# Kernel optimization log

Measured on AMD Instinct MI355X. Metric: run time of the kernel, lower is better.

Reference implementation:

```python
import jax, jax.numpy as jnp
import numpy as np

S_SRC, S_TGT, B = 64, 48, 2048
SRC, TGT, E, H = 256, 256, 512, 1024
NEG = -1e30  # stands in for -inf mask on pad/start classes (identical softmax in fp32)


def setup_inputs() -> dict:
    key = jax.random.key(0)
    ks = jax.random.split(key, 16)
    def p(k, shape):
        return jax.random.normal(k, shape, jnp.float32) * 0.02
    # padding_idx=0 -> embedding row 0 is zeros
    enc_emb = p(ks[0], (SRC, E)).at[0].set(0.0)
    dec_emb = p(ks[1], (TGT, E)).at[0].set(0.0)
    return {
        "src_seq": jax.random.randint(ks[2], (S_SRC, B), 1, SRC),
        "tgt_seq": jax.random.randint(ks[3], (S_TGT, B), 2, TGT),
        "enc_emb": enc_emb,
        "enc_Wih": p(ks[4], (3 * H, E)),
        "enc_Whh": p(ks[5], (3 * H, H)),
        "enc_bih": p(ks[6], (3 * H,)),
        "enc_bhh": p(ks[7], (3 * H,)),
        "dec_emb": dec_emb,
        "dec_Wih": p(ks[8], (3 * H, E)),
        "dec_Whh": p(ks[9], (3 * H, H)),
        "dec_bih": p(ks[10], (3 * H,)),
        "dec_bhh": p(ks[11], (3 * H,)),
        "unemb_W": p(ks[12], (TGT - 2, H)),
        "unemb_b": p(ks[13], (TGT - 2,)),
    }


def gru(x, h0, Wih, Whh, bih, bhh):
    """PyTorch-convention GRU. x: [S,B,E], h0: [B,H]. Gate order r,z,n."""
    xp = jnp.einsum('sbe,ge->sbg', x, Wih) + bih  # input projections for all steps
    def step(h, xt):
        gh = h @ Whh.T + bhh
        xr, xz, xn = jnp.split(xt, 3, axis=-1)
        hr, hz, hn = jnp.split(gh, 3, axis=-1)
        r = jax.nn.sigmoid(xr + hr)
        z = jax.nn.sigmoid(xz + hz)
        n = jnp.tanh(xn + r * hn)
        h = (1 - z) * n + z * h
        return h, h
    hT, hs = jax.lax.scan(step, h0, xp)
    return hs, hT  # [S,B,H], [B,H]


def reference(src_seq, tgt_seq, enc_emb, enc_Wih, enc_Whh, enc_bih, enc_bhh,
              dec_emb, dec_Wih, dec_Whh, dec_bih, dec_bhh, unemb_W, unemb_b):
    # ---- Encoder ----
    x0 = enc_emb[src_seq]                                   # [S_src, B, E]
    h0 = jnp.zeros((src_seq.shape[1], H), x0.dtype)
    _, h = gru(x0, h0, enc_Wih, enc_Whh, enc_bih, enc_bhh)  # [B, H]
    # ---- Decoder (training / teacher-forced path) ----
    xd = dec_emb[tgt_seq]                                   # [S_tgt, B, E]
    xs, _ = gru(xd, h, dec_Wih, dec_Whh, dec_bih, dec_bhh)  # [S_tgt, B, H]
    seq_out = jnp.einsum('sbh,vh->sbv', xs, unemb_W) + unemb_b  # [S_tgt, B, TGT-2]
    mask_cols = jnp.full(seq_out.shape[:-1] + (2,), NEG, seq_out.dtype)
    logits = jnp.concatenate([mask_cols, seq_out], axis=-1)     # [S_tgt, B, TGT]
    # labels shifted left by one; last position = 0 (ignore_index)
    labels = jnp.concatenate([tgt_seq[1:], jnp.zeros_like(tgt_seq[:1])], axis=0)
    logp = jax.nn.log_softmax(logits, axis=-1)
    nll = -jnp.take_along_axis(logp, labels[..., None], axis=-1)[..., 0]
    valid = (labels != 0).astype(nll.dtype)
    return jnp.sum(nll * valid) / jnp.sum(valid)
```

## Files before the change

### kernel.cpp

```cpp
#include <hip/hip_runtime.h>
#include <math.h>

typedef unsigned short ushort_t;
typedef __attribute__((ext_vector_type(8))) short short8;
typedef __attribute__((ext_vector_type(4))) float f32x4;

#define Bn 2048
#define Hn 1024
#define En 512
#define NSLOT 9

__device__ __forceinline__ float sigmoidf_(float x) { return 1.f / (1.f + expf(-x)); }

__device__ __forceinline__ ushort_t bf16rn(float f) {
  unsigned u = __float_as_uint(f);
  return (ushort_t)((u + 0x7FFFu + ((u >> 16) & 1u)) >> 16);
}

__device__ __forceinline__ float bf2f(ushort_t u) {
  return __uint_as_float(((unsigned)u) << 16);
}

__global__ __launch_bounds__(256) void cvt_bf16_kernel(const float* __restrict__ in,
                                                       ushort_t* __restrict__ out, int n4) {
  int i = blockIdx.x * 256 + threadIdx.x;
  if (i < n4) {
    float4 v = ((const float4*)in)[i];
    ushort4 o;
    o.x = bf16rn(v.x); o.y = bf16rn(v.y); o.z = bf16rn(v.z); o.w = bf16rn(v.w);
    ((ushort4*)out)[i] = o;
  }
}

__global__ __launch_bounds__(256) void cvt_pad_wu_kernel(const float* __restrict__ src,
                                                         ushort_t* __restrict__ dst) {
  int i = blockIdx.x * 256 + threadIdx.x;
  if (i < 256 * Hn / 4) {
    float4 v = make_float4(0.f, 0.f, 0.f, 0.f);
    if (i * 4 < 254 * Hn) v = ((const float4*)src)[i];
    ushort4 o;
    o.x = bf16rn(v.x); o.y = bf16rn(v.y); o.z = bf16rn(v.z); o.w = bf16rn(v.w);
    ((ushort4*)dst)[i] = o;
  }
}

#define GLOAD(gsrc, ldst)                                                      \
  __builtin_amdgcn_global_load_lds(                                            \
      (const __attribute__((address_space(1))) unsigned int*)(gsrc),           \
      (__attribute__((address_space(3))) unsigned int*)(ldst), 16, 0, 0)

#define PIPE_BAR(N)                                                            \
  asm volatile("s_waitcnt vmcnt(" #N ")" ::: "memory");                        \
  __builtin_amdgcn_s_barrier();                                                \
  __builtin_amdgcn_sched_barrier(0);

#define SWZ(ROW, C) ((C) ^ (((ROW) >> 1) & 3))
#define SWZ64(ROW, C) ((C) ^ ((ROW) & 7))

__global__ __launch_bounds__(256) void pgemm_kernel(
    const ushort_t* __restrict__ A,
    const ushort_t* __restrict__ Bw,
    const float* __restrict__ bias,
    float* __restrict__ P)
{
  __shared__ __align__(16) ushort_t As[64 * 32];
  __shared__ __align__(16) ushort_t Bs[64 * 32];

  const int tid = threadIdx.x;
  const int lane = tid & 63;
  const int wid = tid >> 6;
  const int wr = wid >> 1, wc = wid & 1;
  const int m0 = blockIdx.x * 64;
  const int n0 = blockIdx.y * 64;

  const int srow = tid >> 2;
  const int sseg = SWZ(srow, tid & 3) * 8;
  const ushort_t* aP = A + (size_t)(m0 + srow) * En + sseg;
  const ushort_t* bP = Bw + (size_t)(n0 + srow) * En + sseg;

  const int kc = lane >> 4;
  const int ra0 = wr * 32 + (lane & 15), ra1 = ra0 + 16;
  const int rb0 = wc * 32 + (lane & 15), rb1 = rb0 + 16;
  const int aoff0 = ra0 * 32 + SWZ(ra0, kc) * 8;
  const int aoff1 = ra1 * 32 + SWZ(ra1, kc) * 8;
  const int boff0 = rb0 * 32 + SWZ(rb0, kc) * 8;
  const int boff1 = rb1 * 32 + SWZ(rb1, kc) * 8;

  const f32x4 zero = {0.f, 0.f, 0.f, 0.f};
  f32x4 acc[2][2] = {{zero, zero}, {zero, zero}};

  for (int k0 = 0; k0 < En; k0 += 32) {
    GLOAD(aP + k0, &As[wid * 512]);
    GLOAD(bP + k0, &Bs[wid * 512]);
    asm volatile("s_waitcnt vmcnt(0)" ::: "memory");
    __syncthreads();
    short8 a0 = *(const short8*)&As[aoff0];
    short8 a1 = *(const short8*)&As[aoff1];
    short8 b0 = *(const short8*)&Bs[boff0];
    short8 b1 = *(const short8*)&Bs[boff1];
    acc[0][0] = __builtin_amdgcn_mfma_f32_16x16x32_bf16(a0, b0, acc[0][0], 0, 0, 0);
    acc[0][1] = __builtin_amdgcn_mfma_f32_16x16x32_bf16(a0, b1, acc[0][1], 0, 0, 0);
    acc[1][0] = __builtin_amdgcn_mfma_f32_16x16x32_bf16(a1, b0, acc[1][0], 0, 0, 0);
    acc[1][1] = __builtin_amdgcn_mfma_f32_16x16x32_bf16(a1, b1, acc[1][1], 0, 0, 0);
    __syncthreads();
  }

  const int colb = n0 + wc * 32 + (lane & 15);
  const int rowb = m0 + wr * 32 + ((lane >> 4) << 2);
#pragma unroll
  for (int j = 0; j < 2; ++j) {
    const int g = colb + j * 16;
    const float bv = bias[g];
#pragma unroll
    for (int i = 0; i < 2; ++i)
#pragma unroll
      for (int reg = 0; reg < 4; ++reg)
        P[(size_t)(rowb + i * 16 + reg) * 3072 + g] = acc[i][j][reg] + bv;
  }
}

#define KSTEP(BUF)                                                             \
  {                                                                            \
    short8 aF[2][2], bF[3][2];                                                 \
    _Pragma("unroll") for (int fi = 0; fi < 2; ++fi)                           \
        _Pragma("unroll") for (int h = 0; h < 2; ++h)                          \
            aF[fi][h] = *(const short8*)&As[BUF][aoff[fi][h]];                 \
    _Pragma("unroll") for (int g = 0; g < 3; ++g)                              \
        _Pragma("unroll") for (int h = 0; h < 2; ++h)                          \
            bF[g][h] = *(const short8*)&Bs[BUF][g][boff[h]];                   \
    __builtin_amdgcn_s_setprio(1);                                             \
    _Pragma("unroll") for (int h = 0; h < 2; ++h)                              \
        _Pragma("unroll") for (int g = 0; g < 3; ++g)                          \
            _Pragma("unroll") for (int fi = 0; fi < 2; ++fi)                   \
                acc[g][fi] = __builtin_amdgcn_mfma_f32_16x16x32_bf16(          \
                    aF[fi][h], bF[g][h], acc[g][fi], 0, 0, 0);                 \
    __builtin_amdgcn_s_setprio(0);                                             \
  }

#define GSTAGE(BUF, T)                                                         \
  {                                                                            \
    const int k0_ = (T) * 64;                                                  \
    GLOAD(aSrc + k0_, &As[BUF][wid * 512]);                                    \
    GLOAD(bSrc0 + k0_, &Bs[BUF][0][wid * 512]);                                \
    GLOAD(bSrc1 + k0_, &Bs[BUF][1][wid * 512]);                                \
    GLOAD(bSrc2 + k0_, &Bs[BUF][2][wid * 512]);                                \
  }

__global__ __launch_bounds__(512, 4) void gru_step_mfma(
    const int* __restrict__ seq_row,
    const float* __restrict__ P,
    const ushort_t* __restrict__ Whh,
    const float* __restrict__ bhh,
    const ushort_t* __restrict__ h_in_b,
    ushort_t* __restrict__ h_out_b)
{
  __shared__ __align__(16) ushort_t As[2][64 * 64];
  __shared__ __align__(16) ushort_t Bs[2][3][64 * 64];
  __shared__ int toks[64];

  const int tid = threadIdx.x;
  const int lane = tid & 63;
  const int wid = tid >> 6;
  const int wr = wid & 1;
  const int wc = wid >> 1;

  const int bid = blockIdx.x;
  const int q = bid & 7, t_ = bid >> 3;
  const int n0 = ((q << 1) | (t_ & 1)) * 64;
  const int m0 = (t_ >> 1) * 64;

  if (tid < 64) toks[tid] = seq_row[m0 + tid];
  __syncthreads();

  const int srow = tid >> 3;
  const int sseg = SWZ64(srow, tid & 7) * 8;

  const ushort_t* aSrc  = h_in_b + (size_t)(m0 + srow) * Hn + sseg;
  const ushort_t* bSrc0 = Whh + (size_t)(0 * Hn + n0 + srow) * Hn + sseg;
  const ushort_t* bSrc1 = Whh + (size_t)(1 * Hn + n0 + srow) * Hn + sseg;
  const ushort_t* bSrc2 = Whh + (size_t)(2 * Hn + n0 + srow) * Hn + sseg;

  const int kc = lane >> 4;
  int aoff[2][2], boff[2];
#pragma unroll
  for (int fi = 0; fi < 2; ++fi) {
    const int ra = wr * 32 + fi * 16 + (lane & 15);
#pragma unroll
    for (int h = 0; h < 2; ++h) aoff[fi][h] = ra * 64 + SWZ64(ra, h * 4 + kc) * 8;
  }
  {
    const int rb = wc * 16 + (lane & 15);
#pragma unroll
    for (int h = 0; h < 2; ++h) boff[h] = rb * 64 + SWZ64(rb, h * 4 + kc) * 8;
  }

  const f32x4 zero = {0.f, 0.f, 0.f, 0.f};
  f32x4 acc[3][2];
#pragma unroll
  for (int g = 0; g < 3; ++g)
#pragma unroll
    for (int fi = 0; fi < 2; ++fi) acc[g][fi] = zero;

  GSTAGE(0, 0);
  int buf = 0;
  for (int t = 0; t < 15; ++t) {
    GSTAGE(buf ^ 1, t + 1);
    PIPE_BAR(4)
    KSTEP(buf)
    buf ^= 1;
  }
  PIPE_BAR(0)
  KSTEP(buf)

  const int n = n0 + wc * 16 + (lane & 15);
  const int rowl = wr * 32 + ((lane >> 4) << 2);
  const float bhr = bhh[n];
  const float bhz = bhh[Hn + n];
  const float bhn = bhh[2 * Hn + n];
#pragma unroll
  for (int fi = 0; fi < 2; ++fi) {
#pragma unroll
    for (int reg = 0; reg < 4; ++reg) {
      const int lr = rowl + fi * 16 + reg;
      const int m = m0 + lr;
      const float* prow = P + (size_t)toks[lr] * 3072;
      const float xr = prow[n];
      const float xz = prow[Hn + n];
      const float xn = prow[2 * Hn + n];
      const float r = sigmoidf_(xr + acc[0][fi][reg] + bhr);
      const float z = sigmoidf_(xz + acc[1][fi][reg] + bhz);
      const float nn = tanhf(xn + r * (acc[2][fi][reg] + bhn));
      const float hv = bf2f(h_in_b[(size_t)m * Hn + n]);
      const float o = (1.f - z) * nn + z * hv;
      h_out_b[(size_t)m * Hn + n] = bf16rn(o);
    }
  }
}

#define USTAGE(BUF, T)                                                         \
  {                                                                            \
    const int k0_ = (T) * 32;                                                  \
    if (uwid < 2) GLOAD(ha + k0_, AsU(BUF) + (tid >> 2) * 32);                 \
    GLOAD(w0 + k0_, BsU(BUF) + 0 * 2048 + uwid * 512);                         \
    GLOAD(w1 + k0_, BsU(BUF) + 1 * 2048 + uwid * 512);                         \
    GLOAD(w2 + k0_, BsU(BUF) + 2 * 2048 + uwid * 512);                         \
    GLOAD(w3 + k0_, BsU(BUF) + 3 * 2048 + uwid * 512);                         \
  }

#define UPIPE_BAR(N01, N23)                                                    \
  {                                                                            \
    if (uwid < 2) { asm volatile("s_waitcnt vmcnt(" #N01 ")" ::: "memory"); }  \
    else          { asm volatile("s_waitcnt vmcnt(" #N23 ")" ::: "memory"); }  \
    __builtin_amdgcn_s_barrier();                                              \
    __builtin_amdgcn_sched_barrier(0);                                         \
  }

#define UKSTEP(BUF)                                                            \
  {                                                                            \
    short8 a_[2], b_[4];                                                       \
    _Pragma("unroll") for (int fi = 0; fi < 2; ++fi)                           \
        a_[fi] = *(const short8*)(AsU(BUF) + uaoff[fi]);                       \
    _Pragma("unroll") for (int fj = 0; fj < 4; ++fj)                           \
        b_[fj] = *(const short8*)(BsU(BUF) + uboff[fj]);                       \
    _Pragma("unroll") for (int fi = 0; fi < 2; ++fi)                           \
        _Pragma("unroll") for (int fj = 0; fj < 4; ++fj)                       \
            acc[fi][fj] = __builtin_amdgcn_mfma_f32_16x16x32_bf16(             \
                a_[fi], b_[fj], acc[fi][fj], 0, 0, 0);                         \
  }

__global__ __launch_bounds__(256) void unembed_batched(
    const ushort_t* __restrict__ hseq,
    int s0,
    const ushort_t* __restrict__ Wp,
    const float* __restrict__ bu,
    const int* __restrict__ tgt_seq,
    double* __restrict__ loss_acc,
    unsigned long long* __restrict__ cnt_acc)
{
  __shared__ __align__(16) char usmem[36 * 1024];
#define AsU(BUF) ((ushort_t*)usmem + (BUF) * 1024)
#define BsU(BUF) ((ushort_t*)(usmem + 4 * 1024) + (BUF) * 8192)
  float* lg = (float*)usmem;

  const int tid = threadIdx.x;
  const int lane = tid & 63;
  const int uwid = tid >> 6;

  const int step = blockIdx.x >> 6;
  const int slot = (s0 + step) % NSLOT;
  const int m0 = (blockIdx.x & 63) * 32;
  const ushort_t* h_b = hseq + (size_t)slot * Bn * Hn;
  const int* labels = tgt_seq + (size_t)(s0 + step + 1) * Bn;

  const int srow = tid >> 2;
  const int sseg = SWZ(srow, tid & 3) * 8;

  const ushort_t* ha = h_b + (size_t)(m0 + srow) * Hn + sseg;
  const ushort_t* w0 = Wp + (size_t)(0 * 64 + srow) * Hn + sseg;
  const ushort_t* w1 = Wp + (size_t)(1 * 64 + srow) * Hn + sseg;
  const ushort_t* w2 = Wp + (size_t)(2 * 64 + srow) * Hn + sseg;
  const ushort_t* w3 = Wp + (size_t)(3 * 64 + srow) * Hn + sseg;

  const int kc = lane >> 4;
  int uaoff[2], uboff[4];
#pragma unroll
  for (int fi = 0; fi < 2; ++fi) {
    const int ra = fi * 16 + (lane & 15);
    uaoff[fi] = ra * 32 + SWZ(ra, kc) * 8;
  }
#pragma unroll
  for (int fj = 0; fj < 4; ++fj) {
    const int rb = uwid * 64 + fj * 16 + (lane & 15);
    uboff[fj] = rb * 32 + SWZ(rb, kc) * 8;
  }

  const f32x4 zero = {0.f, 0.f, 0.f, 0.f};
  f32x4 acc[2][4];
#pragma unroll
  for (int fi = 0; fi < 2; ++fi)
#pragma unroll
    for (int fj = 0; fj < 4; ++fj) acc[fi][fj] = zero;

  USTAGE(0, 0);
  int buf = 0;
  for (int t = 0; t < 31; ++t) {
    USTAGE(buf ^ 1, t + 1);
    UPIPE_BAR(5, 4)
    UKSTEP(buf)
    buf ^= 1;
  }
  UPIPE_BAR(0, 0)
  UKSTEP(buf)

  __syncthreads();
#pragma unroll
  for (int fj = 0; fj < 4; ++fj) {
    const int col = uwid * 64 + fj * 16 + (lane & 15);
    const float bv = (col < 254) ? bu[col] : 0.f;
#pragma unroll
    for (int fi = 0; fi < 2; ++fi) {
#pragma unroll
      for (int reg = 0; reg < 4; ++reg) {
        const int row = fi * 16 + (lane >> 4) * 4 + reg;
        lg[row * 256 + col] = (col < 254) ? (acc[fi][fj][reg] + bv) : -1e30f;
      }
    }
  }
  __syncthreads();

  float wsum = 0.f;
  int wcnt = 0;
#pragma unroll
  for (int rr = 0; rr < 8; ++rr) {
    const int r = uwid * 8 + rr;
    const float4 v4 = *(const float4*)&lg[r * 256 + lane * 4];
    float mx = fmaxf(fmaxf(v4.x, v4.y), fmaxf(v4.z, v4.w));
    for (int o = 32; o > 0; o >>= 1) mx = fmaxf(mx, __shfl_xor(mx, o));
    float s = expf(v4.x - mx) + expf(v4.y - mx) + expf(v4.z - mx) + expf(v4.w - mx);
    for (int o = 32; o > 0; o >>= 1) s += __shfl_xor(s, o);
    if (lane == 0) {
      const int lab = labels[m0 + r];
      if (lab != 0) {
        wsum += (logf(s) + mx) - lg[r * 256 + lab - 2];
        wcnt += 1;
      }
    }
  }
  if (lane == 0) {
    atomicAdd(loss_acc, (double)wsum);
    atomicAdd(cnt_acc, (unsigned long long)wcnt);
  }
}

__global__ void finalize_kernel(const double* __restrict__ loss_acc,
                                const unsigned long long* __restrict__ cnt_acc,
                                unsigned* __restrict__ out)
{
  unsigned long long cnt = cnt_acc[0];
  if (cnt == 0ull) cnt = 1ull;
  const float f = (float)(loss_acc[0] / (double)cnt);
  const unsigned u = __float_as_uint(f);
  const unsigned bf = (u + 0x7FFFu + ((u >> 16) & 1u)) >> 16;
  out[0] = (u & 0xFFFF0000u) | (bf & 0xFFFFu);
}

extern "C" void kernel_launch(void* const* d_in, const int* in_sizes, int n_in,
                              void* d_out, int out_size, void* d_ws, size_t ws_size,
                              hipStream_t stream)
{
  const int* src_seq = (const int*)d_in[0];
  const int* tgt_seq = (const int*)d_in[1];
  const float* enc_emb = (const float*)d_in[2];
  const float* enc_Wih = (const float*)d_in[3];
  const float* enc_Whh = (const float*)d_in[4];
  const float* enc_bih = (const float*)d_in[5];
  const float* enc_bhh = (const float*)d_in[6];
  const float* dec_emb = (const float*)d_in[7];
  const float* dec_Wih = (const float*)d_in[8];
  const float* dec_Whh = (const float*)d_in[9];
  const float* dec_bih = (const float*)d_in[10];
  const float* dec_bhh = (const float*)d_in[11];
  const float* unemb_W = (const float*)d_in[12];
  const float* unemb_b = (const float*)d_in[13];

  char* p = (char*)d_ws;
  ushort_t* hseq = (ushort_t*)p; p += (size_t)NSLOT * Bn * Hn * 2;
  ushort_t* eWih = (ushort_t*)p; p += (size_t)3 * Hn * En * 2;
  ushort_t* eWhh = (ushort_t*)p; p += (size_t)3 * Hn * Hn * 2;
  ushort_t* dWih = (ushort_t*)p; p += (size_t)3 * Hn * En * 2;
  ushort_t* dWhh = (ushort_t*)p; p += (size_t)3 * Hn * Hn * 2;
  ushort_t* eEmb = (ushort_t*)p; p += (size_t)256 * En * 2;
  ushort_t* dEmb = (ushort_t*)p; p += (size_t)256 * En * 2;
  ushort_t* Wp   = (ushort_t*)p; p += (size_t)256 * Hn * 2;
  float* Pe = (float*)p; p += (size_t)256 * 3072 * 4;
  float* Pd = (float*)p; p += (size_t)256 * 3072 * 4;
  double* loss_acc = (double*)p;
  unsigned long long* cnt_acc = (unsigned long long*)(p + 8);

  ushort_t* slot7 = hseq + (size_t)7 * Bn * Hn;
  ushort_t* slot8 = hseq + (size_t)8 * Bn * Hn;

  hipMemsetAsync(slot7, 0, (size_t)Bn * Hn * 2, stream);
  hipMemsetAsync(loss_acc, 0, 16, stream);

  struct { const float* src; ushort_t* dst; int n; } cv[6] = {
      {enc_Wih, eWih, 3 * Hn * En}, {enc_Whh, eWhh, 3 * Hn * Hn},
      {dec_Wih, dWih, 3 * Hn * En}, {dec_Whh, dWhh, 3 * Hn * Hn},
      {enc_emb, eEmb, 256 * En},    {dec_emb, dEmb, 256 * En}};
  for (int i = 0; i < 6; ++i) {
    int n4 = cv[i].n / 4;
    cvt_bf16_kernel<<<(n4 + 255) / 256, 256, 0, stream>>>(cv[i].src, cv[i].dst, n4);
  }
  cvt_pad_wu_kernel<<<(256 * Hn / 4 + 255) / 256, 256, 0, stream>>>(unemb_W, Wp);

  {
    const dim3 pg(4, 48);
    pgemm_kernel<<<pg, 256, 0, stream>>>(eEmb, eWih, enc_bih, Pe);
    pgemm_kernel<<<pg, 256, 0, stream>>>(dEmb, dWih, dec_bih, Pd);
  }

  const ushort_t* in_b = slot7;
  for (int s = 0; s < 64; ++s) {
    ushort_t* out_b = (s & 1) ? slot7 : slot8;
    gru_step_mfma<<<512, 512, 0, stream>>>(src_seq + (size_t)s * Bn, Pe, eWhh, enc_bhh,
                                           in_b, out_b);
    in_b = out_b;
  }

  int done = 0;
  for (int s = 0; s < 47; ++s) {
    const ushort_t* din_b = (s == 0) ? slot7 : hseq + (size_t)((s - 1) % NSLOT) * Bn * Hn;
    ushort_t* dout_b = hseq + (size_t)(s % NSLOT) * Bn * Hn;
    gru_step_mfma<<<512, 512, 0, stream>>>(tgt_seq + (size_t)s * Bn, Pd, dWhh, dec_bhh,
                                           din_b, dout_b);
    if (s == 7 || s == 15 || s == 23 || s == 31 || s == 39 || s == 46) {
      const int cnt = s + 1 - done;
      unembed_batched<<<cnt * 64, 256, 0, stream>>>(hseq, done, Wp, unemb_b, tgt_seq,
                                                    loss_acc, cnt_acc);
      done = s + 1;
    }
  }

  finalize_kernel<<<1, 1, 0, stream>>>(loss_acc, cnt_acc, (unsigned*)d_out);
}
```

Baseline: 2.593 ms.

## Process two timesteps per unembed block with 64-wide K tiles and 8 waves

The unembedding kernel now handles a pair of decoder timesteps per block (64 rows of h), using 512 threads arranged as 2x4 waves and a K-tile of 64 instead of 32. Each staged slice of the weight matrix is therefore reused across twice as many rows, and there are half as many pipeline iterations and barriers. It also raises MFMA priority with s_setprio and skips atomics from waves with no contributions. The cost is higher LDS use (80KB) per block, fewer blocks in flight, and an odd-count tail where half the block does redundant work.

```diff
diff --git a/kernel.cpp b/kernel.cpp
--- a/kernel.cpp
+++ b/kernel.cpp
@@ -239,79 +239,83 @@
 
 #define USTAGE(BUF, T)                                                         \
   {                                                                            \
-    const int k0_ = (T) * 32;                                                  \
-    if (uwid < 2) GLOAD(ha + k0_, AsU(BUF) + (tid >> 2) * 32);                 \
-    GLOAD(w0 + k0_, BsU(BUF) + 0 * 2048 + uwid * 512);                         \
-    GLOAD(w1 + k0_, BsU(BUF) + 1 * 2048 + uwid * 512);                         \
-    GLOAD(w2 + k0_, BsU(BUF) + 2 * 2048 + uwid * 512);                         \
-    GLOAD(w3 + k0_, BsU(BUF) + 3 * 2048 + uwid * 512);                         \
-  }
-
-#define UPIPE_BAR(N01, N23)                                                    \
-  {                                                                            \
-    if (uwid < 2) { asm volatile("s_waitcnt vmcnt(" #N01 ")" ::: "memory"); }  \
-    else          { asm volatile("s_waitcnt vmcnt(" #N23 ")" ::: "memory"); }  \
-    __builtin_amdgcn_s_barrier();                                              \
-    __builtin_amdgcn_sched_barrier(0);                                         \
+    const int k0_ = (T) * 64;                                                  \
+    GLOAD(ha + k0_, AsU(BUF) + wid * 512);                                     \
+    GLOAD(w0 + k0_, BsU(BUF) + 0 * 4096 + wid * 512);                          \
+    GLOAD(w1 + k0_, BsU(BUF) + 1 * 4096 + wid * 512);                          \
+    GLOAD(w2 + k0_, BsU(BUF) + 2 * 4096 + wid * 512);                          \
+    GLOAD(w3 + k0_, BsU(BUF) + 3 * 4096 + wid * 512);                          \
   }
 
 #define UKSTEP(BUF)                                                            \
   {                                                                            \
-    short8 a_[2], b_[4];                                                       \
+    short8 a_[2][2], b_[4][2];                                                 \
     _Pragma("unroll") for (int fi = 0; fi < 2; ++fi)                           \
-        a_[fi] = *(const short8*)(AsU(BUF) + uaoff[fi]);                       \
+        _Pragma("unroll") for (int h = 0; h < 2; ++h)                          \
+            a_[fi][h] = *(const short8*)(AsU(BUF) + uaoff[fi][h]);             \
     _Pragma("unroll") for (int fj = 0; fj < 4; ++fj)                           \
-        b_[fj] = *(const short8*)(BsU(BUF) + uboff[fj]);                       \
-    _Pragma("unroll") for (int fi = 0; fi < 2; ++fi)                           \
-        _Pragma("unroll") for (int fj = 0; fj < 4; ++fj)                       \
-            acc[fi][fj] = __builtin_amdgcn_mfma_f32_16x16x32_bf16(             \
-                a_[fi], b_[fj], acc[fi][fj], 0, 0, 0);                         \
-  }
-
-__global__ __launch_bounds__(256) void unembed_batched(
+        _Pragma("unroll") for (int h = 0; h < 2; ++h)                          \
+            b_[fj][h] = *(const short8*)(BsU(BUF) + uboff[fj][h]);             \
+    __builtin_amdgcn_s_setprio(1);                                             \
+    _Pragma("unroll") for (int h = 0; h < 2; ++h)                              \
+        _Pragma("unroll") for (int fi = 0; fi < 2; ++fi)                       \
+            _Pragma("unroll") for (int fj = 0; fj < 4; ++fj)                   \
+                acc[fi][fj] = __builtin_amdgcn_mfma_f32_16x16x32_bf16(         \
+                    a_[fi][h], b_[fj][h], acc[fi][fj], 0, 0, 0);               \
+    __builtin_amdgcn_s_setprio(0);                                             \
+  }
+
+__global__ __launch_bounds__(512) void unembed_batched(
     const ushort_t* __restrict__ hseq,
-    int s0,
+    int s0, int scnt,
     const ushort_t* __restrict__ Wp,
     const float* __restrict__ bu,
     const int* __restrict__ tgt_seq,
     double* __restrict__ loss_acc,
     unsigned long long* __restrict__ cnt_acc)
 {
-  __shared__ __align__(16) char usmem[36 * 1024];
-#define AsU(BUF) ((ushort_t*)usmem + (BUF) * 1024)
-#define BsU(BUF) ((ushort_t*)(usmem + 4 * 1024) + (BUF) * 8192)
+  __shared__ __align__(16) char usmem[80 * 1024];
+#define AsU(BUF) ((ushort_t*)usmem + (BUF) * 4096)
+#define BsU(BUF) ((ushort_t*)(usmem + 16 * 1024) + (BUF) * 16384)
   float* lg = (float*)usmem;
 
   const int tid = threadIdx.x;
   const int lane = tid & 63;
-  const int uwid = tid >> 6;
-
-  const int step = blockIdx.x >> 6;
-  const int slot = (s0 + step) % NSLOT;
+  const int wid = tid >> 6;
+  const int wr = wid >> 2;
+  const int wc = wid & 3;
+
+  const int pair = blockIdx.x >> 6;
   const int m0 = (blockIdx.x & 63) * 32;
-  const ushort_t* h_b = hseq + (size_t)slot * Bn * Hn;
-  const int* labels = tgt_seq + (size_t)(s0 + step + 1) * Bn;
-
-  const int srow = tid >> 2;
-  const int sseg = SWZ(srow, tid & 3) * 8;
-
-  const ushort_t* ha = h_b + (size_t)(m0 + srow) * Hn + sseg;
+  const int sA = s0 + 2 * pair;
+  const int has2 = (2 * pair + 1) < scnt;
+  const int slotA = sA % NSLOT;
+  const int slotB = has2 ? (sA + 1) % NSLOT : slotA;
+
+  const int srow = tid >> 3;
+  const int sseg = SWZ64(srow, tid & 7) * 8;
+
+  const ushort_t* hbase =
+      hseq + (size_t)(srow < 32 ? slotA : slotB) * Bn * Hn;
+  const ushort_t* ha = hbase + (size_t)(m0 + (srow & 31)) * Hn + sseg;
   const ushort_t* w0 = Wp + (size_t)(0 * 64 + srow) * Hn + sseg;
   const ushort_t* w1 = Wp + (size_t)(1 * 64 + srow) * Hn + sseg;
   const ushort_t* w2 = Wp + (size_t)(2 * 64 + srow) * Hn + sseg;
   const ushort_t* w3 = Wp + (size_t)(3 * 64 + srow) * Hn + sseg;
 
   const int kc = lane >> 4;
-  int uaoff[2], uboff[4];
+  int uaoff[2][2], uboff[4][2];
 #pragma unroll
   for (int fi = 0; fi < 2; ++fi) {
-    const int ra = fi * 16 + (lane & 15);
-    uaoff[fi] = ra * 32 + SWZ(ra, kc) * 8;
+    const int ra = wr * 32 + fi * 16 + (lane & 15);
+#pragma unroll
+    for (int h = 0; h < 2; ++h) uaoff[fi][h] = ra * 64 + SWZ64(ra, h * 4 + kc) * 8;
   }
 #pragma unroll
   for (int fj = 0; fj < 4; ++fj) {
-    const int rb = uwid * 64 + fj * 16 + (lane & 15);
-    uboff[fj] = rb * 32 + SWZ(rb, kc) * 8;
+    const int rb = wc * 64 + fj * 16 + (lane & 15);
+#pragma unroll
+    for (int h = 0; h < 2; ++h) uboff[fj][h] = rb * 64 + SWZ64(rb, h * 4 + kc) * 8;
   }
 
   const f32x4 zero = {0.f, 0.f, 0.f, 0.f};
@@ -323,25 +327,25 @@
 
   USTAGE(0, 0);
   int buf = 0;
-  for (int t = 0; t < 31; ++t) {
+  for (int t = 0; t < 15; ++t) {
     USTAGE(buf ^ 1, t + 1);
-    UPIPE_BAR(5, 4)
+    PIPE_BAR(5)
     UKSTEP(buf)
     buf ^= 1;
   }
-  UPIPE_BAR(0, 0)
+  PIPE_BAR(0)
   UKSTEP(buf)
 
   __syncthreads();
 #pragma unroll
   for (int fj = 0; fj < 4; ++fj) {
-    const int col = uwid * 64 + fj * 16 + (lane & 15);
+    const int col = wc * 64 + fj * 16 + (lane & 15);
     const float bv = (col < 254) ? bu[col] : 0.f;
 #pragma unroll
     for (int fi = 0; fi < 2; ++fi) {
 #pragma unroll
       for (int reg = 0; reg < 4; ++reg) {
-        const int row = fi * 16 + (lane >> 4) * 4 + reg;
+        const int row = wr * 32 + fi * 16 + (lane >> 4) * 4 + reg;
         lg[row * 256 + col] = (col < 254) ? (acc[fi][fj][reg] + bv) : -1e30f;
       }
     }
@@ -350,23 +354,27 @@
 
   float wsum = 0.f;
   int wcnt = 0;
-#pragma unroll
-  for (int rr = 0; rr < 8; ++rr) {
-    const int r = uwid * 8 + rr;
-    const float4 v4 = *(const float4*)&lg[r * 256 + lane * 4];
-    float mx = fmaxf(fmaxf(v4.x, v4.y), fmaxf(v4.z, v4.w));
-    for (int o = 32; o > 0; o >>= 1) mx = fmaxf(mx, __shfl_xor(mx, o));
-    float s = expf(v4.x - mx) + expf(v4.y - mx) + expf(v4.z - mx) + expf(v4.w - mx);
-    for (int o = 32; o > 0; o >>= 1) s += __shfl_xor(s, o);
-    if (lane == 0) {
-      const int lab = labels[m0 + r];
-      if (lab != 0) {
-        wsum += (logf(s) + mx) - lg[r * 256 + lab - 2];
-        wcnt += 1;
+  if (wid < 4 || has2) {
+    const int isB = (wid >= 4);
+    const int* labels = tgt_seq + (size_t)(sA + 1 + isB) * Bn;
+#pragma unroll
+    for (int rr = 0; rr < 8; ++rr) {
+      const int r = wid * 8 + rr;
+      const float4 v4 = *(const float4*)&lg[r * 256 + lane * 4];
+      float mx = fmaxf(fmaxf(v4.x, v4.y), fmaxf(v4.z, v4.w));
+      for (int o = 32; o > 0; o >>= 1) mx = fmaxf(mx, __shfl_xor(mx, o));
+      float s = expf(v4.x - mx) + expf(v4.y - mx) + expf(v4.z - mx) + expf(v4.w - mx);
+      for (int o = 32; o > 0; o >>= 1) s += __shfl_xor(s, o);
+      if (lane == 0) {
+        const int lab = labels[m0 + (r & 31)];
+        if (lab != 0) {
+          wsum += (logf(s) + mx) - lg[r * 256 + lab - 2];
+          wcnt += 1;
+        }
       }
     }
   }
-  if (lane == 0) {
+  if (lane == 0 && wcnt > 0) {
     atomicAdd(loss_acc, (double)wsum);
     atomicAdd(cnt_acc, (unsigned long long)wcnt);
   }
@@ -455,8 +463,9 @@
                                            din_b, dout_b);
     if (s == 7 || s == 15 || s == 23 || s == 31 || s == 39 || s == 46) {
       const int cnt = s + 1 - done;
-      unembed_batched<<<cnt * 64, 256, 0, stream>>>(hseq, done, Wp, unemb_b, tgt_seq,
-                                                    loss_acc, cnt_acc);
+      const int npair = (cnt + 1) / 2;
+      unembed_batched<<<npair * 64, 512, 0, stream>>>(hseq, done, cnt, Wp, unemb_b,
+                                                      tgt_seq, loss_acc, cnt_acc);
       done = s + 1;
     }
   }
```

After: 2.582 ms. No clear change (-0.4%).
